# Optimization experiments

Hardware: AMD Instinct MI355X
Metric: run time of the kernel (lower is better)

The kernel has to match this reference:

```python
import jax, jax.numpy as jnp
import numpy as np

N_DELTA, N_THETA, N_GAMMA = 8, 16, 64
HIDDEN = 64
N_STEPS = 20
DT = 0.01
K_INTRA = 1.0   # within-band Kuramoto coupling
K_CROSS = 0.5   # slow-band -> fast-band drive
TWO_PI = 2.0 * np.pi


def _lin(key, fan_in, fan_out):
    s = 1.0 / np.sqrt(fan_in)
    kw, kb = jax.random.split(key)
    w = jax.random.uniform(kw, (fan_in, fan_out), jnp.float32, -s, s)
    b = jax.random.uniform(kb, (fan_out,), jnp.float32, -s, s)
    return w, b


def setup_inputs() -> dict:
    key = jax.random.key(0)
    ks = jax.random.split(key, 12)
    B, N, D_SCENE, D_QUERY = 65536, 8, 16, 60
    scene = jax.random.normal(ks[0], (B, N, D_SCENE), jnp.float32)
    query = jax.random.normal(ks[1], (B, D_QUERY), jnp.float32)
    # per-sample seeded initial oscillator state (phases uniform, band-typical freqs in Hz)
    delta_phase0 = jax.random.uniform(ks[2], (B, N_DELTA), jnp.float32, 0.0, TWO_PI)
    theta_phase0 = jax.random.uniform(ks[3], (B, N_THETA), jnp.float32, 0.0, TWO_PI)
    gamma_phase0 = jax.random.uniform(ks[4], (B, N_GAMMA), jnp.float32, 0.0, TWO_PI)
    delta_freq = jax.random.uniform(ks[5], (B, N_DELTA), jnp.float32, 1.0, 4.0)
    theta_freq = jax.random.uniform(ks[6], (B, N_THETA), jnp.float32, 4.0, 8.0)
    gamma_freq = jax.random.uniform(ks[7], (B, N_GAMMA), jnp.float32, 30.0, 80.0)
    scene_w, scene_b = _lin(ks[8], D_SCENE, N_GAMMA)
    query_w, query_b = _lin(ks[9], D_QUERY, HIDDEN)
    total_osc = N_DELTA + N_THETA + N_GAMMA
    ro_w1, ro_b1 = _lin(ks[10], total_osc + HIDDEN, HIDDEN)
    ro_w2, ro_b2 = _lin(ks[11], HIDDEN, 2)
    return dict(scene=scene, query=query,
                delta_phase0=delta_phase0, theta_phase0=theta_phase0, gamma_phase0=gamma_phase0,
                delta_freq=delta_freq, theta_freq=theta_freq, gamma_freq=gamma_freq,
                scene_w=scene_w, scene_b=scene_b, query_w=query_w, query_b=query_b,
                ro_w1=ro_w1, ro_b1=ro_b1, ro_w2=ro_w2, ro_b2=ro_b2)


def _meanfield(p, a):
    # mean_j a_j*sin(p_j - p_i) computed in O(n) via sin/cos decomposition
    s = jnp.mean(a * jnp.sin(p), axis=-1, keepdims=True)
    c = jnp.mean(a * jnp.cos(p), axis=-1, keepdims=True)
    return jnp.cos(p) * s - jnp.sin(p) * c


def _cross(p_slow, a_slow, p_fast):
    s = jnp.mean(a_slow * jnp.sin(p_slow), axis=-1, keepdims=True)
    c = jnp.mean(a_slow * jnp.cos(p_slow), axis=-1, keepdims=True)
    return jnp.cos(p_fast) * s - jnp.sin(p_fast) * c


def _integrate(pd, ad, pt, at, pg, ag, fd, ft, fg):
    def step(carry, _):
        pd, ad, pt, at, pg, ag = carry
        dpd = TWO_PI * fd + K_INTRA * _meanfield(pd, ad)
        dpt = TWO_PI * ft + K_INTRA * _meanfield(pt, at) + K_CROSS * _cross(pd, ad, pt)
        dpg = TWO_PI * fg + K_INTRA * _meanfield(pg, ag) + K_CROSS * _cross(pt, at, pg)
        dad = ad * (1.0 - ad * ad)   # Stuart-Landau amplitude relaxation
        dat = at * (1.0 - at * at)
        dag = ag * (1.0 - ag * ag)
        new = (pd + DT * dpd, ad + DT * dad,
               pt + DT * dpt, at + DT * dat,
               pg + DT * dpg, ag + DT * dag)
        return new, None
    (pd, ad, pt, at, pg, ag), _ = jax.lax.scan(step, (pd, ad, pt, at, pg, ag), None, length=N_STEPS)
    return ad, at, ag


def reference(scene, query, delta_phase0, theta_phase0, gamma_phase0,
              delta_freq, theta_freq, gamma_freq,
              scene_w, scene_b, query_w, query_b, ro_w1, ro_b1, ro_w2, ro_b2):
    scene_flat = jnp.mean(scene, axis=1)                       # (B, D_scene)
    gamma_init = jax.nn.sigmoid(scene_flat @ scene_w + scene_b)  # (B, n_gamma)
    gamma_init = jax.lax.stop_gradient(gamma_init)             # .detach() in original
    B = scene.shape[0]
    ad0 = jnp.ones((B, N_DELTA), scene.dtype)
    at0 = jnp.ones((B, N_THETA), scene.dtype)
    ad, at, ag = _integrate(delta_phase0, ad0, theta_phase0, at0,
                            gamma_phase0, gamma_init,
                            delta_freq, theta_freq, gamma_freq)
    osc_feat = jnp.concatenate([ad, at, ag], axis=-1)          # (B, 88)
    q_feat = query @ query_w + query_b                         # (B, hidden)
    combined = jnp.concatenate([osc_feat, q_feat], axis=-1)    # (B, 152)
    h = jax.nn.relu(combined @ ro_w1 + ro_b1)
    logits = h @ ro_w2 + ro_b2
    return jax.nn.log_softmax(logits, axis=-1)
```

## Files before the change

kernel.cpp:

```cpp
#include <hip/hip_runtime.h>


#define WS_WQ    0
#define WS_BEFF  3840

__global__ __launch_bounds__(256) void dtg_prep(
    const float* __restrict__ qw, const float* __restrict__ qb,
    const float* __restrict__ w1, const float* __restrict__ b1,
    float* __restrict__ ws)
{
  __shared__ float sm[256];
  const int blk = blockIdx.x, tid = threadIdx.x;
  const int c = tid & 63, p = tid >> 6;
  if (blk < 60) {
    float acc = 0.f;
    for (int j = p * 16; j < p * 16 + 16; ++j)
      acc = fmaf(qw[blk * 64 + j], w1[(88 + j) * 64 + c], acc);
    sm[tid] = acc;
    __syncthreads();
    if (tid < 64)
      ws[WS_WQ + blk * 64 + tid] = sm[tid] + sm[64 + tid] + sm[128 + tid] + sm[192 + tid];
  } else {
    float acc = 0.f;
    if (p == 0) {
      acc = b1[c];
      for (int r = 0; r < 24; ++r) acc += w1[r * 64 + c];
    }
    for (int j = p * 16; j < p * 16 + 16; ++j)
      acc = fmaf(qb[j], w1[(88 + j) * 64 + c], acc);
    sm[tid] = acc;
    __syncthreads();
    if (tid < 64)
      ws[WS_BEFF + tid] = sm[tid] + sm[64 + tid] + sm[128 + tid] + sm[192 + tid];
  }
}

#define L_X2   0
#define L_SF   (124 * 68)
#define L_TOT  (L_SF + 16 * 68)

#define KSTEP(ACC, XV, WV)                                                     \
  { const float x_[4] = {(XV).x, (XV).y, (XV).z, (XV).w};                      \
    const float w_[4] = {(WV).x, (WV).y, (WV).z, (WV).w};                      \
    _Pragma("unroll") for (int si_ = 0; si_ < 4; ++si_)                        \
      _Pragma("unroll") for (int ci_ = 0; ci_ < 4; ++ci_)                      \
        ACC[si_][ci_] = fmaf(x_[si_], w_[ci_], ACC[si_][ci_]); }

__global__ __launch_bounds__(256, 4) void dtg_main(
    const float* __restrict__ scene,
    const float* __restrict__ query,
    const float* __restrict__ sw,
    const float* __restrict__ sb,
    const float* __restrict__ w1,
    const float* __restrict__ w2,
    const float* __restrict__ b2,
    const float* __restrict__ ws,
    float* __restrict__ outf)
{
  __shared__ float lds[L_TOT];
  const int tid = threadIdx.x;
  const int blk = blockIdx.x;

  {
    const int s = tid >> 2, q = tid & 3;
    const float4* sp = (const float4*)scene + (size_t)blk * 2048;
    float4 a = make_float4(0.f, 0.f, 0.f, 0.f);
#pragma unroll
    for (int n = 0; n < 8; ++n) {
      float4 v = sp[s * 32 + n * 4 + q];
      a.x += v.x; a.y += v.y; a.z += v.z; a.w += v.w;
    }
    lds[L_SF + (4 * q + 0) * 68 + s] = a.x * 0.125f;
    lds[L_SF + (4 * q + 1) * 68 + s] = a.y * 0.125f;
    lds[L_SF + (4 * q + 2) * 68 + s] = a.z * 0.125f;
    lds[L_SF + (4 * q + 3) * 68 + s] = a.w * 0.125f;

    const float4* qp = (const float4*)query + (size_t)blk * 960;
#pragma unroll
    for (int m = 0; m < 4; ++m) {
      int f4i = q + 4 * m;
      if (f4i < 15) {
        float4 v = qp[s * 15 + f4i];
        int k0 = 4 * f4i;
        lds[L_X2 + (k0 + 0) * 68 + s] = v.x;
        lds[L_X2 + (k0 + 1) * 68 + s] = v.y;
        lds[L_X2 + (k0 + 2) * 68 + s] = v.z;
        lds[L_X2 + (k0 + 3) * 68 + s] = v.w;
      }
    }
  }
  __syncthreads();

  const int sgrp = tid >> 4, cgrp = tid & 15;
  const float4* swp = (const float4*)sw;
  const float4* wqp = (const float4*)(ws + WS_WQ);
  const float4* w1p = (const float4*)(w1 + 24 * 64);

  float ga[4][4];
  {
    float4 bsv = ((const float4*)sb)[cgrp];
#pragma unroll
    for (int si = 0; si < 4; ++si) {
      ga[si][0] = bsv.x; ga[si][1] = bsv.y; ga[si][2] = bsv.z; ga[si][3] = bsv.w;
    }
#pragma unroll 4
    for (int k = 0; k < 16; ++k) {
      float4 xv = *(const float4*)(lds + L_SF + k * 68 + 4 * sgrp);
      float4 wv = swp[k * 16 + cgrp];
      KSTEP(ga, xv, wv)
    }
  }

#pragma unroll
  for (int si = 0; si < 4; ++si)
#pragma unroll
    for (int ci = 0; ci < 4; ++ci)
      ga[si][ci] = __builtin_amdgcn_rcpf(1.f + __expf(-ga[si][ci]));
  for (int t = 0; t < 20; ++t) {
#pragma unroll
    for (int si = 0; si < 4; ++si)
#pragma unroll
      for (int ci = 0; ci < 4; ++ci) {
        float a = ga[si][ci];
        ga[si][ci] = fmaf(0.01f, a - a * a * a, a);
      }
  }

#pragma unroll
  for (int ci = 0; ci < 4; ++ci) {
    float4 gw = make_float4(ga[0][ci], ga[1][ci], ga[2][ci], ga[3][ci]);
    *(float4*)(lds + L_X2 + (60 + 4 * cgrp + ci) * 68 + 4 * sgrp) = gw;
  }
  __syncthreads();

  float ha[4][4];
  {
    float4 bev = *(const float4*)(ws + WS_BEFF + 4 * cgrp);
#pragma unroll
    for (int si = 0; si < 4; ++si) {
      ha[si][0] = bev.x; ha[si][1] = bev.y; ha[si][2] = bev.z; ha[si][3] = bev.w;
    }
#pragma unroll 4
    for (int k = 0; k < 60; ++k) {
      float4 xv = *(const float4*)(lds + L_X2 + k * 68 + 4 * sgrp);
      float4 wv = wqp[k * 16 + cgrp];
      KSTEP(ha, xv, wv)
    }
#pragma unroll 4
    for (int k = 0; k < 64; ++k) {
      float4 xv = *(const float4*)(lds + L_X2 + (60 + k) * 68 + 4 * sgrp);
      float4 wv = w1p[k * 16 + cgrp];
      KSTEP(ha, xv, wv)
    }
  }

  float l0[4], l1[4];
  {
    float2 w2c[4];
#pragma unroll
    for (int ci = 0; ci < 4; ++ci)
      w2c[ci] = ((const float2*)w2)[4 * cgrp + ci];
#pragma unroll
    for (int si = 0; si < 4; ++si) {
      float a0 = 0.f, a1 = 0.f;
#pragma unroll
      for (int ci = 0; ci < 4; ++ci) {
        float r = fmaxf(ha[si][ci], 0.f);
        a0 = fmaf(r, w2c[ci].x, a0);
        a1 = fmaf(r, w2c[ci].y, a1);
      }
      l0[si] = a0; l1[si] = a1;
    }
  }
#pragma unroll
  for (int m = 1; m < 16; m <<= 1) {
#pragma unroll
    for (int si = 0; si < 4; ++si) {
      l0[si] += __shfl_xor(l0[si], m);
      l1[si] += __shfl_xor(l1[si], m);
    }
  }
  if (cgrp == 0) {
    const float bb0 = b2[0], bb1 = b2[1];
    const int base = blk * 64 + 4 * sgrp;
    float r[8];
#pragma unroll
    for (int si = 0; si < 4; ++si) {
      float a0 = l0[si] + bb0, a1 = l1[si] + bb1;
      float mx  = fmaxf(a0, a1);
      float e0  = __expf(a0 - mx), e1 = __expf(a1 - mx);
      float lse = mx + __logf(e0 + e1);
      r[2 * si] = a0 - lse; r[2 * si + 1] = a1 - lse;
    }
    float4* op = (float4*)(outf + 2 * base);
    op[0] = make_float4(r[0], r[1], r[2], r[3]);
    op[1] = make_float4(r[4], r[5], r[6], r[7]);
  }
}

extern "C" void kernel_launch(void* const* d_in, const int* in_sizes, int n_in,
                              void* d_out, int out_size, void* d_ws, size_t ws_size,
                              hipStream_t stream)
{
  const float* scene = (const float*)d_in[0];
  const float* query = (const float*)d_in[1];
  const float* sw = (const float*)d_in[8];
  const float* sb = (const float*)d_in[9];
  const float* qw = (const float*)d_in[10];
  const float* qb = (const float*)d_in[11];
  const float* w1 = (const float*)d_in[12];
  const float* b1 = (const float*)d_in[13];
  const float* w2 = (const float*)d_in[14];
  const float* b2 = (const float*)d_in[15];
  float* ws = (float*)d_ws;
  const int B = in_sizes[0] / 128;

  hipLaunchKernelGGL(dtg_prep, dim3(61), dim3(256), 0, stream,
                     qw, qb, w1, b1, ws);
  hipLaunchKernelGGL(dtg_main, dim3(B / 64), dim3(256), 0, stream,
                     scene, query, sw, sb, w1, w2, b2, ws, (float*)d_out);
}
```

Baseline: 153.2 us.

## Compute readout hidden layer with split-bf16 MFMA instead of scalar FMA

Replaces the per-thread fp32 FMA loops for the 124x64 hidden-layer GEMM with bf16 MFMA 16x16x32 instructions. Precision is kept by splitting activations and weights into high and low bf16 parts (hi*hi + hi*lo + lo*hi). A new single-block prep kernel pre-packs the fused weights into MFMA fragment layout in workspace. This adds a third launch and some conversion work on activations, and drops the occupancy hint from launch bounds.

```diff
diff --git a/kernel.cpp b/kernel.cpp
--- a/kernel.cpp
+++ b/kernel.cpp
@@ -1,8 +1,21 @@
 #include <hip/hip_runtime.h>
 
+
+typedef __attribute__((ext_vector_type(8))) short short8;
+typedef __attribute__((ext_vector_type(4))) float f32x4;
+
+__device__ __forceinline__ unsigned short f2bf(float f) {
+  unsigned u = __float_as_uint(f);
+  return (unsigned short)((u + 0x7FFFu + ((u >> 16) & 1u)) >> 16);
+}
+__device__ __forceinline__ float bf2f(unsigned short s) {
+  return __uint_as_float(((unsigned)s) << 16);
+}
 
 #define WS_WQ    0
 #define WS_BEFF  3840
+#define WS_WHF   3904
+#define WS_WLF   8000
 
 __global__ __launch_bounds__(256) void dtg_prep(
     const float* __restrict__ qw, const float* __restrict__ qb,
@@ -35,9 +48,37 @@
   }
 }
 
-#define L_X2   0
-#define L_SF   (124 * 68)
-#define L_TOT  (L_SF + 16 * 68)
+__global__ __launch_bounds__(256) void dtg_prep2(
+    const float* __restrict__ w1, float* __restrict__ ws)
+{
+  const int tid = threadIdx.x;
+  unsigned short* dh = (unsigned short*)(ws + WS_WHF);
+  unsigned short* dl = (unsigned short*)(ws + WS_WLF);
+  for (int it = 0; it < 4; ++it) {
+    const int idx  = it * 256 + tid;
+    const int frag = idx >> 6, lane = idx & 63;
+    const int nt = frag >> 2, kk = frag & 3;
+    const int n = nt * 16 + (lane & 15), q = lane >> 4;
+    unsigned short hh[8], ll[8];
+#pragma unroll
+    for (int j = 0; j < 8; ++j) {
+      const int k = kk * 32 + q * 8 + j;
+      float w;
+      if      (k < 60)  w = ws[WS_WQ + k * 64 + n];
+      else if (k < 124) w = w1[(24 + k - 60) * 64 + n];
+      else              w = 0.f;
+      hh[j] = f2bf(w);
+      ll[j] = f2bf(w - bf2f(hh[j]));
+    }
+#pragma unroll
+    for (int j = 0; j < 8; ++j) { dh[idx * 8 + j] = hh[j]; dl[idx * 8 + j] = ll[j]; }
+  }
+}
+
+#define XH_OFF 0
+#define XL_OFF 17408
+#define SF_OFF 26624
+#define L_BYTES (26624 + 16*68*4)
 
 #define KSTEP(ACC, XV, WV)                                                     \
   { const float x_[4] = {(XV).x, (XV).y, (XV).z, (XV).w};                      \
@@ -46,20 +87,20 @@
       _Pragma("unroll") for (int ci_ = 0; ci_ < 4; ++ci_)                      \
         ACC[si_][ci_] = fmaf(x_[si_], w_[ci_], ACC[si_][ci_]); }
 
-__global__ __launch_bounds__(256, 4) void dtg_main(
+__global__ __launch_bounds__(256) void dtg_main(
     const float* __restrict__ scene,
     const float* __restrict__ query,
     const float* __restrict__ sw,
     const float* __restrict__ sb,
-    const float* __restrict__ w1,
     const float* __restrict__ w2,
     const float* __restrict__ b2,
     const float* __restrict__ ws,
     float* __restrict__ outf)
 {
-  __shared__ float lds[L_TOT];
+  __shared__ __align__(16) char smem[L_BYTES];
   const int tid = threadIdx.x;
   const int blk = blockIdx.x;
+  float* sf = (float*)(smem + SF_OFF);
 
   {
     const int s = tid >> 2, q = tid & 3;
@@ -70,131 +111,144 @@
       float4 v = sp[s * 32 + n * 4 + q];
       a.x += v.x; a.y += v.y; a.z += v.z; a.w += v.w;
     }
-    lds[L_SF + (4 * q + 0) * 68 + s] = a.x * 0.125f;
-    lds[L_SF + (4 * q + 1) * 68 + s] = a.y * 0.125f;
-    lds[L_SF + (4 * q + 2) * 68 + s] = a.z * 0.125f;
-    lds[L_SF + (4 * q + 3) * 68 + s] = a.w * 0.125f;
+    sf[(4 * q + 0) * 68 + s] = a.x * 0.125f;
+    sf[(4 * q + 1) * 68 + s] = a.y * 0.125f;
+    sf[(4 * q + 2) * 68 + s] = a.z * 0.125f;
+    sf[(4 * q + 3) * 68 + s] = a.w * 0.125f;
 
     const float4* qp = (const float4*)query + (size_t)blk * 960;
 #pragma unroll
     for (int m = 0; m < 4; ++m) {
-      int f4i = q + 4 * m;
+      const int f4i = q + 4 * m;
       if (f4i < 15) {
         float4 v = qp[s * 15 + f4i];
-        int k0 = 4 * f4i;
-        lds[L_X2 + (k0 + 0) * 68 + s] = v.x;
-        lds[L_X2 + (k0 + 1) * 68 + s] = v.y;
-        lds[L_X2 + (k0 + 2) * 68 + s] = v.z;
-        lds[L_X2 + (k0 + 3) * 68 + s] = v.w;
+        const float xs[4] = {v.x, v.y, v.z, v.w};
+        unsigned short h[4], l[4];
+#pragma unroll
+        for (int j = 0; j < 4; ++j) {
+          h[j] = f2bf(xs[j]);
+          l[j] = f2bf(xs[j] - bf2f(h[j]));
+        }
+        uint2 ph, pl;
+        ph.x = (unsigned)h[0] | ((unsigned)h[1] << 16);
+        ph.y = (unsigned)h[2] | ((unsigned)h[3] << 16);
+        pl.x = (unsigned)l[0] | ((unsigned)l[1] << 16);
+        pl.y = (unsigned)l[2] | ((unsigned)l[3] << 16);
+        *(uint2*)(smem + XH_OFF + s * 272 + f4i * 8) = ph;
+        *(uint2*)(smem + XL_OFF + s * 144 + f4i * 8) = pl;
       }
     }
+    if (tid < 64) {
+      *(uint2*)(smem + XH_OFF + tid * 272 + 248) = make_uint2(0u, 0u);
+      *(uint2*)(smem + XL_OFF + tid * 144 + 120) = make_uint2(0u, 0u);
+    }
   }
   __syncthreads();
 
   const int sgrp = tid >> 4, cgrp = tid & 15;
-  const float4* swp = (const float4*)sw;
-  const float4* wqp = (const float4*)(ws + WS_WQ);
-  const float4* w1p = (const float4*)(w1 + 24 * 64);
-
-  float ga[4][4];
   {
+    float ga[4][4];
     float4 bsv = ((const float4*)sb)[cgrp];
 #pragma unroll
     for (int si = 0; si < 4; ++si) {
       ga[si][0] = bsv.x; ga[si][1] = bsv.y; ga[si][2] = bsv.z; ga[si][3] = bsv.w;
     }
+    const float4* swp = (const float4*)sw;
 #pragma unroll 4
     for (int k = 0; k < 16; ++k) {
-      float4 xv = *(const float4*)(lds + L_SF + k * 68 + 4 * sgrp);
+      float4 xv = *(const float4*)(sf + k * 68 + 4 * sgrp);
       float4 wv = swp[k * 16 + cgrp];
       KSTEP(ga, xv, wv)
     }
-  }
-
-#pragma unroll
-  for (int si = 0; si < 4; ++si)
-#pragma unroll
-    for (int ci = 0; ci < 4; ++ci)
-      ga[si][ci] = __builtin_amdgcn_rcpf(1.f + __expf(-ga[si][ci]));
-  for (int t = 0; t < 20; ++t) {
 #pragma unroll
     for (int si = 0; si < 4; ++si)
 #pragma unroll
-      for (int ci = 0; ci < 4; ++ci) {
-        float a = ga[si][ci];
-        ga[si][ci] = fmaf(0.01f, a - a * a * a, a);
-      }
-  }
-
-#pragma unroll
-  for (int ci = 0; ci < 4; ++ci) {
-    float4 gw = make_float4(ga[0][ci], ga[1][ci], ga[2][ci], ga[3][ci]);
-    *(float4*)(lds + L_X2 + (60 + 4 * cgrp + ci) * 68 + 4 * sgrp) = gw;
+      for (int ci = 0; ci < 4; ++ci)
+        ga[si][ci] = __builtin_amdgcn_rcpf(1.f + __expf(-ga[si][ci]));
+    for (int st = 0; st < 20; ++st) {
+#pragma unroll
+      for (int si = 0; si < 4; ++si)
+#pragma unroll
+        for (int ci = 0; ci < 4; ++ci) {
+          float a = ga[si][ci];
+          ga[si][ci] = fmaf(0.01f, a - a * a * a, a);
+        }
+    }
+#pragma unroll
+    for (int si = 0; si < 4; ++si) {
+      uint2 pw;
+      pw.x = (unsigned)f2bf(ga[si][0]) | ((unsigned)f2bf(ga[si][1]) << 16);
+      pw.y = (unsigned)f2bf(ga[si][2]) | ((unsigned)f2bf(ga[si][3]) << 16);
+      *(uint2*)(smem + XH_OFF + (4 * sgrp + si) * 272 + 120 + 8 * cgrp) = pw;
+    }
   }
   __syncthreads();
 
-  float ha[4][4];
-  {
-    float4 bev = *(const float4*)(ws + WS_BEFF + 4 * cgrp);
-#pragma unroll
-    for (int si = 0; si < 4; ++si) {
-      ha[si][0] = bev.x; ha[si][1] = bev.y; ha[si][2] = bev.z; ha[si][3] = bev.w;
-    }
-#pragma unroll 4
-    for (int k = 0; k < 60; ++k) {
-      float4 xv = *(const float4*)(lds + L_X2 + k * 68 + 4 * sgrp);
-      float4 wv = wqp[k * 16 + cgrp];
-      KSTEP(ha, xv, wv)
-    }
-#pragma unroll 4
-    for (int k = 0; k < 64; ++k) {
-      float4 xv = *(const float4*)(lds + L_X2 + (60 + k) * 68 + 4 * sgrp);
-      float4 wv = w1p[k * 16 + cgrp];
-      KSTEP(ha, xv, wv)
-    }
-  }
-
-  float l0[4], l1[4];
-  {
-    float2 w2c[4];
-#pragma unroll
-    for (int ci = 0; ci < 4; ++ci)
-      w2c[ci] = ((const float2*)w2)[4 * cgrp + ci];
-#pragma unroll
-    for (int si = 0; si < 4; ++si) {
-      float a0 = 0.f, a1 = 0.f;
-#pragma unroll
-      for (int ci = 0; ci < 4; ++ci) {
-        float r = fmaxf(ha[si][ci], 0.f);
-        a0 = fmaf(r, w2c[ci].x, a0);
-        a1 = fmaf(r, w2c[ci].y, a1);
-      }
-      l0[si] = a0; l1[si] = a1;
+  const int wv   = tid >> 6, lane = tid & 63;
+  const int quad = lane >> 4;
+  const int mrow = wv * 16 + (lane & 15);
+  const char* arow = smem + XH_OFF + mrow * 272 + quad * 16;
+  short8 Ah0 = *(const short8*)(arow + 0);
+  short8 Ah1 = *(const short8*)(arow + 64);
+  short8 Ah2 = *(const short8*)(arow + 128);
+  short8 Ah3 = *(const short8*)(arow + 192);
+  const char* lrow = smem + XL_OFF + mrow * 144 + quad * 16;
+  short8 Al0 = *(const short8*)(lrow + 0);
+  short8 Al1 = *(const short8*)(lrow + 64);
+
+  const short8* Bh = (const short8*)(ws + WS_WHF);
+  const short8* Bl = (const short8*)(ws + WS_WLF);
+
+  float l0[4] = {0.f, 0.f, 0.f, 0.f}, l1[4] = {0.f, 0.f, 0.f, 0.f};
+#pragma unroll
+  for (int nt = 0; nt < 4; ++nt) {
+    const short8* bh = Bh + (nt * 4) * 64 + lane;
+    const short8* bl = Bl + (nt * 4) * 64 + lane;
+    f32x4 acc = {0.f, 0.f, 0.f, 0.f};
+    acc = __builtin_amdgcn_mfma_f32_16x16x32_bf16(Ah0, bh[0],   acc, 0, 0, 0);
+    acc = __builtin_amdgcn_mfma_f32_16x16x32_bf16(Ah1, bh[64],  acc, 0, 0, 0);
+    acc = __builtin_amdgcn_mfma_f32_16x16x32_bf16(Ah2, bh[128], acc, 0, 0, 0);
+    acc = __builtin_amdgcn_mfma_f32_16x16x32_bf16(Ah3, bh[192], acc, 0, 0, 0);
+    acc = __builtin_amdgcn_mfma_f32_16x16x32_bf16(Ah0, bl[0],   acc, 0, 0, 0);
+    acc = __builtin_amdgcn_mfma_f32_16x16x32_bf16(Ah1, bl[64],  acc, 0, 0, 0);
+    acc = __builtin_amdgcn_mfma_f32_16x16x32_bf16(Ah2, bl[128], acc, 0, 0, 0);
+    acc = __builtin_amdgcn_mfma_f32_16x16x32_bf16(Ah3, bl[192], acc, 0, 0, 0);
+    acc = __builtin_amdgcn_mfma_f32_16x16x32_bf16(Al0, bh[0],   acc, 0, 0, 0);
+    acc = __builtin_amdgcn_mfma_f32_16x16x32_bf16(Al1, bh[64],  acc, 0, 0, 0);
+
+    const int col = nt * 16 + (lane & 15);
+    const float be = ws[WS_BEFF + col];
+    const float2 w2v = ((const float2*)w2)[col];
+#pragma unroll
+    for (int r = 0; r < 4; ++r) {
+      float h = fmaxf(acc[r] + be, 0.f);
+      l0[r] = fmaf(h, w2v.x, l0[r]);
+      l1[r] = fmaf(h, w2v.y, l1[r]);
     }
   }
 #pragma unroll
   for (int m = 1; m < 16; m <<= 1) {
 #pragma unroll
-    for (int si = 0; si < 4; ++si) {
-      l0[si] += __shfl_xor(l0[si], m);
-      l1[si] += __shfl_xor(l1[si], m);
-    }
-  }
-  if (cgrp == 0) {
+    for (int r = 0; r < 4; ++r) {
+      l0[r] += __shfl_xor(l0[r], m);
+      l1[r] += __shfl_xor(l1[r], m);
+    }
+  }
+  if ((lane & 15) == 0) {
     const float bb0 = b2[0], bb1 = b2[1];
-    const int base = blk * 64 + 4 * sgrp;
-    float r[8];
-#pragma unroll
-    for (int si = 0; si < 4; ++si) {
-      float a0 = l0[si] + bb0, a1 = l1[si] + bb1;
+    float rr[8];
+#pragma unroll
+    for (int r = 0; r < 4; ++r) {
+      float a0 = l0[r] + bb0, a1 = l1[r] + bb1;
       float mx  = fmaxf(a0, a1);
       float e0  = __expf(a0 - mx), e1 = __expf(a1 - mx);
       float lse = mx + __logf(e0 + e1);
-      r[2 * si] = a0 - lse; r[2 * si + 1] = a1 - lse;
-    }
-    float4* op = (float4*)(outf + 2 * base);
-    op[0] = make_float4(r[0], r[1], r[2], r[3]);
-    op[1] = make_float4(r[4], r[5], r[6], r[7]);
+      rr[2 * r] = a0 - lse; rr[2 * r + 1] = a1 - lse;
+    }
+    const int base = blk * 64 + wv * 16 + quad * 4;
+    float4* op = (float4*)(outf + base * 2);
+    op[0] = make_float4(rr[0], rr[1], rr[2], rr[3]);
+    op[1] = make_float4(rr[4], rr[5], rr[6], rr[7]);
   }
 }
 
@@ -215,8 +269,8 @@
   float* ws = (float*)d_ws;
   const int B = in_sizes[0] / 128;
 
-  hipLaunchKernelGGL(dtg_prep, dim3(61), dim3(256), 0, stream,
-                     qw, qb, w1, b1, ws);
-  hipLaunchKernelGGL(dtg_main, dim3(B / 64), dim3(256), 0, stream,
-                     scene, query, sw, sb, w1, w2, b2, ws, (float*)d_out);
-}
+  hipLaunchKernelGGL(dtg_prep,  dim3(61), dim3(256), 0, stream, qw, qb, w1, b1, ws);
+  hipLaunchKernelGGL(dtg_prep2, dim3(1),  dim3(256), 0, stream, w1, ws);
+  hipLaunchKernelGGL(dtg_main,  dim3(B / 64), dim3(256), 0, stream,
+                     scene, query, sw, sb, w2, b2, ws, (float*)d_out);
+}
```

Measured after the change: 147.7 us. -3.6%, faster.
